# Kernel tuning notes

Measured on AMD Instinct MI355X. Metric: run time of the kernel, lower is better.

Reference implementation:

```python
import jax, jax.numpy as jnp
import numpy as np

B, N, D = 8, 2048, 1024


def setup_inputs() -> dict:
    key = jax.random.key(0)
    k = jax.random.split(key, 6)
    scale = 1.0 / np.sqrt(D)
    x = jax.random.normal(k[0], (B, N, D), dtype=jnp.float32)
    attention_mask = jax.random.randint(k[1], (B, N, N), 0, 2, dtype=jnp.int32)
    W_qkv = jax.random.normal(k[2], (D, 3 * D), dtype=jnp.float32) * scale
    b_qkv = jax.random.normal(k[3], (3 * D,), dtype=jnp.float32) * 0.01
    W_out = jax.random.normal(k[4], (D, D), dtype=jnp.float32) * scale
    b_out = jax.random.normal(k[5], (D,), dtype=jnp.float32) * 0.01
    return {"x": x, "attention_mask": attention_mask, "W_qkv": W_qkv,
            "b_qkv": b_qkv, "W_out": W_out, "b_out": b_out}


def reference(x, attention_mask, W_qkv, b_qkv, W_out, b_out):
    # QKV projection: [B,N,3D]
    qkv = jnp.einsum('bnd,de->bne', x, W_qkv) + b_qkv
    Q, K, V = jnp.split(qkv, 3, axis=-1)
    inv_sqrt_d = jnp.float32(1.0 / np.sqrt(D))
    # naive full [B,N,N] attention scores
    scores = jnp.einsum('bqd,bkd->bqk', Q, K) * inv_sqrt_d
    w = jax.nn.softmax(scores, axis=-1)
    # masked_fill(mask == 0, -1e20) then renormalize (module applies softmax
    # again over the masked weights; dropout is identity in eval mode)
    w = jnp.where(attention_mask == 0, jnp.float32(-1e20), w)
    w = jax.nn.softmax(w, axis=-1)
    out = jnp.einsum('bqk,bkd->bqd', w, V)
    return jnp.einsum('bnd,de->bne', out, W_out) + b_out
```

## Files before the change

kernel.cpp:

```cpp
#include <hip/hip_runtime.h>
#include <hip/hip_bf16.h>

typedef __attribute__((ext_vector_type(8))) short short8;
typedef __attribute__((ext_vector_type(4))) float floatx4;
typedef __attribute__((ext_vector_type(8))) int intx8;

#define AS_GLOBAL(p) ((const __attribute__((address_space(1))) void*)(p))
#define AS_LOCAL(p)  ((__attribute__((address_space(3))) void*)(p))

__device__ __forceinline__ float b2f(unsigned short u) {
    union { unsigned int u; float f; } c; c.u = ((unsigned int)u) << 16; return c.f;
}
__device__ __forceinline__ unsigned short f2b(float f) {
    union { float f; unsigned int u; } c; c.f = f;
    unsigned int u = c.u;
    unsigned int r = (u + 0x7fffu + ((u >> 16) & 1u)) >> 16;
    return (unsigned short)r;
}
__device__ __forceinline__ unsigned char f2fp8(float v) {
    return (unsigned char)(__builtin_amdgcn_cvt_pk_fp8_f32(v, v, 0, false) & 0xff);
}

__global__ __launch_bounds__(256) void cast_x(
    const float* __restrict__ in, unsigned short* __restrict__ xbf,
    unsigned int* __restrict__ xf8, int n4) {
    int i = blockIdx.x * 256 + threadIdx.x;
    if (i >= n4) return;
    float4 v = ((const float4*)in)[i];
    ushort4 o;
    o.x = f2b(v.x); o.y = f2b(v.y); o.z = f2b(v.z); o.w = f2b(v.w);
    ((ushort4*)xbf)[i] = o;
    int p = __builtin_amdgcn_cvt_pk_fp8_f32(v.x, v.y, 0, false);
    p = __builtin_amdgcn_cvt_pk_fp8_f32(v.z, v.w, p, true);
    xf8[i] = (unsigned int)p;
}

__global__ __launch_bounds__(256) void transpose_f32_bf16(
    const float* __restrict__ in, unsigned short* __restrict__ out, int R, int C) {
    __shared__ float t[32][33];
    int c0 = blockIdx.x * 32, r0 = blockIdx.y * 32;
    int tx = threadIdx.x, ty = threadIdx.y;
#pragma unroll
    for (int k = 0; k < 32; k += 8)
        t[ty + k][tx] = in[(size_t)(r0 + ty + k) * C + c0 + tx];
    __syncthreads();
#pragma unroll
    for (int k = 0; k < 32; k += 8)
        out[(size_t)(c0 + ty + k) * R + r0 + tx] = f2b(t[tx][ty + k]);
}

__global__ __launch_bounds__(256) void transpose_f32_fp8_qk(
    const float* __restrict__ in, unsigned char* __restrict__ out) {
    __shared__ float t[32][33];
    int c0 = blockIdx.x * 32, r0 = blockIdx.y * 32;
    int tx = threadIdx.x, ty = threadIdx.y;
#pragma unroll
    for (int k = 0; k < 32; k += 8)
        t[ty + k][tx] = in[(size_t)(r0 + ty + k) * 3072 + c0 + tx];
    __syncthreads();
#pragma unroll
    for (int k = 0; k < 32; k += 8)
        out[(size_t)(c0 + ty + k) * 1024 + r0 + tx] = f2fp8(t[tx][ty + k]);
}

__global__ __launch_bounds__(256) void cast_wv(
    const float* __restrict__ in, unsigned short* __restrict__ out) {
    int i = blockIdx.x * 256 + threadIdx.x;
    int d = i >> 8, rem = (i & 255) * 4;
    float4 v = *(const float4*)&in[(size_t)d * 3072 + 2048 + rem];
    ushort4 o;
    o.x = f2b(v.x); o.y = f2b(v.y); o.z = f2b(v.z); o.w = f2b(v.w);
    *(ushort4*)&out[(size_t)d * 1024 + rem] = o;
}

__global__ __launch_bounds__(256) void bvo_kernel(
    const unsigned short* __restrict__ WoT, const float* __restrict__ bqkv,
    const float* __restrict__ bout, float* __restrict__ bvo) {
    int wv = threadIdx.x >> 6, lane = threadIdx.x & 63;
    int e = blockIdx.x * 4 + wv;
    const unsigned short* row = WoT + (size_t)e * 1024;
    float s = 0.f;
    for (int h = lane; h < 1024; h += 64) s += b2f(row[h]) * bqkv[2048 + h];
#pragma unroll
    for (int o = 32; o; o >>= 1) s += __shfl_xor(s, o);
    if (lane == 0) bvo[e] = s + bout[e];
}

__global__ __launch_bounds__(256) void softmax2_kernel(
    unsigned short* __restrict__ S, const int* __restrict__ mask) {
    const int N = 2048;
    int wv = threadIdx.x >> 6, lane = threadIdx.x & 63;
    size_t row = (size_t)blockIdx.x * 4 + wv;
    unsigned short* srow = S + row * N;
    const int* mrow = mask + row * N;

    float e1[32];
    float l = 0.f;
#pragma unroll
    for (int i = 0; i < 4; ++i) {
        uint4 raw = ((const uint4*)srow)[lane + 64 * i];
        unsigned v[4] = { raw.x, raw.y, raw.z, raw.w };
#pragma unroll
        for (int j = 0; j < 4; ++j) {
            float a = b2f((unsigned short)(v[j] & 0xffff));
            float bb = b2f((unsigned short)(v[j] >> 16));
            float ea = __expf(a), eb = __expf(bb);
            e1[i * 8 + 2 * j] = ea; e1[i * 8 + 2 * j + 1] = eb;
            l += ea + eb;
        }
    }
#pragma unroll
    for (int o = 32; o; o >>= 1) l += __shfl_xor(l, o);
    float invl = 1.0f / l;

    float e2[32];
    float z = 0.f;
#pragma unroll
    for (int i = 0; i < 4; ++i) {
        uint4 m0 = ((const uint4*)mrow)[2 * (lane + 64 * i)];
        uint4 m1 = ((const uint4*)mrow)[2 * (lane + 64 * i) + 1];
        int mk[8] = { (int)m0.x, (int)m0.y, (int)m0.z, (int)m0.w,
                      (int)m1.x, (int)m1.y, (int)m1.z, (int)m1.w };
#pragma unroll
        for (int j = 0; j < 8; ++j) {
            float w1 = e1[i * 8 + j] * invl;
            float e = mk[j] ? __expf(w1) : 0.0f;
            e2[i * 8 + j] = e; z += e;
        }
    }
#pragma unroll
    for (int o = 32; o; o >>= 1) z += __shfl_xor(z, o);
    float invz = (z > 0.f) ? 1.0f / z : 0.0f;
    float fallback = 1.0f / N;
#pragma unroll
    for (int i = 0; i < 4; ++i) {
        float p[8];
#pragma unroll
        for (int j = 0; j < 8; ++j)
            p[j] = (z > 0.f) ? e2[i * 8 + j] * invz : fallback;
        uint4 o;
        o.x = (unsigned)f2b(p[0]) | ((unsigned)f2b(p[1]) << 16);
        o.y = (unsigned)f2b(p[2]) | ((unsigned)f2b(p[3]) << 16);
        o.z = (unsigned)f2b(p[4]) | ((unsigned)f2b(p[5]) << 16);
        o.w = (unsigned)f2b(p[6]) | ((unsigned)f2b(p[7]) << 16);
        ((uint4*)srow)[lane + 64 * i] = o;
    }
}

template <int TAG, bool BIAS, int OUT, int XS, int YS>
__global__ __launch_bounds__(256) void gemm_bt(
    const unsigned short* __restrict__ A, int ldA, long long strideA,
    const unsigned short* __restrict__ B, int ldB, long long strideB,
    void* __restrict__ C, int ldC, long long strideC,
    const float* __restrict__ bias, float scale, int K) {
    __shared__ __align__(16) unsigned short lds[2 * 128 * 64];
    unsigned short* At = lds;
    unsigned short* Bt = lds + 128 * 64;

    unsigned flat = blockIdx.x;
    unsigned wg = (flat & 7u) * (gridDim.x >> 3) + (flat >> 3);
    int bx = wg & ((1u << XS) - 1u);
    int by = (wg >> XS) & ((1u << YS) - 1u);
    int bz = wg >> (XS + YS);

    const unsigned short* Ab = A + (size_t)bz * strideA;
    const unsigned short* Bb = B + (size_t)bz * strideB;
    int tn0 = bx * 128;
    int tm0 = by * 128;
    int tid = threadIdx.x;
    int wave = tid >> 6, lane = tid & 63;
    int lm = lane & 15, q = lane >> 4;
    int wm = (wave >> 1) * 64, wn = (wave & 1) * 64;

    int srow = lane >> 3;
    int sblk = lane & 7;

    floatx4 acc[4][4] = {};

    for (int k0 = 0; k0 < K; k0 += 64) {
        __syncthreads();
#pragma unroll
        for (int i = 0; i < 4; ++i) {
            int chunk = wave * 4 + i;
            int r = chunk * 8 + srow;
            int blk = sblk ^ (r & 7);
            const unsigned short* ga = Ab + (size_t)(tm0 + r) * ldA + (k0 + blk * 8);
            __builtin_amdgcn_global_load_lds(AS_GLOBAL(ga), AS_LOCAL(At + chunk * 512), 16, 0, 0);
            const unsigned short* gb = Bb + (size_t)(tn0 + r) * ldB + (k0 + blk * 8);
            __builtin_amdgcn_global_load_lds(AS_GLOBAL(gb), AS_LOCAL(Bt + chunk * 512), 16, 0, 0);
        }
        __syncthreads();
#pragma unroll
        for (int kk = 0; kk < 2; ++kk) {
            short8 af[4], bf[4];
#pragma unroll
            for (int mt = 0; mt < 4; ++mt) {
                int r = wm + mt * 16 + lm;
                af[mt] = *(const short8*)(At + r * 64 + (((kk * 4 + q) ^ (r & 7)) * 8));
            }
#pragma unroll
            for (int nt = 0; nt < 4; ++nt) {
                int r = wn + nt * 16 + lm;
                bf[nt] = *(const short8*)(Bt + r * 64 + (((kk * 4 + q) ^ (r & 7)) * 8));
            }
#pragma unroll
            for (int mt = 0; mt < 4; ++mt)
#pragma unroll
                for (int nt = 0; nt < 4; ++nt)
                    acc[mt][nt] = __builtin_amdgcn_mfma_f32_16x16x32_bf16(
                        af[mt], bf[nt], acc[mt][nt], 0, 0, 0);
        }
    }

    float biasv[4];
#pragma unroll
    for (int nt = 0; nt < 4; ++nt)
        biasv[nt] = BIAS ? bias[tn0 + wn + nt * 16 + lm] : 0.0f;

    if (OUT == 2) {
        __syncthreads();
        unsigned short* T = lds;
#pragma unroll
        for (int mt = 0; mt < 4; ++mt)
#pragma unroll
            for (int nt = 0; nt < 4; ++nt) {
                int n = wn + nt * 16 + lm;
                int m0 = wm + mt * 16 + q * 4;
                int col = m0 ^ ((n & 15) << 3);
                ushort4 pv;
                float v0 = acc[mt][nt][0] * scale; if (BIAS) v0 += biasv[nt];
                float v1 = acc[mt][nt][1] * scale; if (BIAS) v1 += biasv[nt];
                float v2 = acc[mt][nt][2] * scale; if (BIAS) v2 += biasv[nt];
                float v3 = acc[mt][nt][3] * scale; if (BIAS) v3 += biasv[nt];
                pv.x = f2b(v0); pv.y = f2b(v1); pv.z = f2b(v2); pv.w = f2b(v3);
                *(ushort4*)&T[n * 128 + col] = pv;
            }
        __syncthreads();
        unsigned short* Cb = (unsigned short*)C + (size_t)(tm0 >> 11) * strideC + (tm0 & 2047);
#pragma unroll
        for (int r8 = 0; r8 < 8; ++r8) {
            int idx = tid + 256 * r8;
            int d = idx >> 4, c = idx & 15;
            int cs = (c ^ (d & 15)) << 3;
            short8 v = *(const short8*)&T[d * 128 + cs];
            *(short8*)&Cb[(size_t)(tn0 + d) * ldC + c * 8] = v;
        }
        return;
    }

#pragma unroll
    for (int mt = 0; mt < 4; ++mt) {
#pragma unroll
        for (int nt = 0; nt < 4; ++nt) {
            int gm = tm0 + wm + mt * 16 + q * 4;
            int gn = tn0 + wn + nt * 16 + lm;
#pragma unroll
            for (int r = 0; r < 4; ++r) {
                float v = acc[mt][nt][r] * scale;
                if (BIAS) v += biasv[nt];
                size_t idx = (size_t)bz * strideC + (size_t)(gm + r) * ldC + gn;
                if (OUT == 1) ((float*)C)[idx] = v;
                else          ((unsigned short*)C)[idx] = f2b(v);
            }
        }
    }
}

template <int MH>
__device__ __forceinline__ void mfma16(floatx4 (&acc)[8][4], const short8 (&af)[4],
                                       const short8 (&bf)[4]) {
#pragma unroll
    for (int m = 0; m < 4; ++m)
#pragma unroll
        for (int n = 0; n < 4; ++n)
            acc[MH * 4 + m][n] = __builtin_amdgcn_mfma_f32_16x16x32_bf16(
                af[m], bf[n], acc[MH * 4 + m][n], 0, 0, 0);
}

template <int NXB, int NYB>
__global__ __launch_bounds__(512, 2) void gemm_bt8(
    const unsigned short* __restrict__ A, int ldA, long long strideA,
    const unsigned short* __restrict__ B, int ldB, long long strideB,
    float* __restrict__ C, int ldC, long long strideC,
    float scale, int K) {
    __shared__ __align__(16) unsigned short lds[65536];
    constexpr int TILE = 16384;
    constexpr int BREG = 32768;

    int tid = threadIdx.x;
    int wave = tid >> 6, lane = tid & 63;
    int lm = lane & 15, q = lane >> 4;
    int wmi = wave >> 2, wni = wave & 3;

    unsigned flat = blockIdx.x;
    unsigned wg = (flat & 7u) * (gridDim.x >> 3) + (flat >> 3);
    int bx = wg % NXB;
    int rem = wg / NXB;
    int by = rem % NYB;
    int bz = rem / NYB;
    int tn0 = bx * 256, tm0 = by * 256;

    const unsigned short* Ab = A + (size_t)bz * strideA;
    const unsigned short* Bb = B + (size_t)bz * strideB;

    int srow8 = lane >> 3, s7 = lane & 7;
    const unsigned short* gA[4];
    const unsigned short* gB[4];
#pragma unroll
    for (int i = 0; i < 4; ++i) {
        int r = i * 64 + wave * 8 + srow8;
        int blk = s7 ^ (r & 7);
        gA[i] = Ab + (size_t)(tm0 + r) * ldA + blk * 8;
        gB[i] = Bb + (size_t)(tn0 + r) * ldB + blk * 8;
    }

    int nt = K >> 6;

#pragma unroll
    for (int i = 0; i < 4; ++i)
        __builtin_amdgcn_global_load_lds(AS_GLOBAL(gB[i]), AS_LOCAL(lds + BREG + i * 4096 + wave * 512), 16, 0, 0);
#pragma unroll
    for (int i = 0; i < 4; ++i)
        __builtin_amdgcn_global_load_lds(AS_GLOBAL(gA[i]), AS_LOCAL(lds + i * 4096 + wave * 512), 16, 0, 0);
#pragma unroll
    for (int i = 0; i < 4; ++i) { gA[i] += 64; gB[i] += 64; }

    asm volatile("s_waitcnt vmcnt(0)" ::: "memory");
    __builtin_amdgcn_s_barrier();

    floatx4 acc[8][4] = {};
    short8 bf0[4], bf1[4];
    short8 af[4];

    int aOff = (wmi * 128 + lm) * 64;
    int bOff = (wni * 64 + lm) * 64;
    int sl0 = (q ^ (lm & 7)) * 8;
    int sl1 = ((4 + q) ^ (lm & 7)) * 8;

    for (int t = 0; t < nt; ++t) {
        unsigned short* Ap = lds + (t & 1) * TILE;
        unsigned short* Bp = lds + BREG + (t & 1) * TILE;
        unsigned short* An = lds + ((t + 1) & 1) * TILE;
        unsigned short* Bn = lds + BREG + ((t + 1) & 1) * TILE;
        bool pre = (t + 1) < nt;

#pragma unroll
        for (int n = 0; n < 4; ++n) bf0[n] = *(const short8*)(Bp + bOff + n * 1024 + sl0);
#pragma unroll
        for (int n = 0; n < 4; ++n) bf1[n] = *(const short8*)(Bp + bOff + n * 1024 + sl1);
#pragma unroll
        for (int m = 0; m < 4; ++m) af[m] = *(const short8*)(Ap + aOff + m * 1024 + sl0);
        if (pre) {
#pragma unroll
            for (int i = 0; i < 4; ++i)
                __builtin_amdgcn_global_load_lds(AS_GLOBAL(gB[i]), AS_LOCAL(Bn + i * 4096 + wave * 512), 16, 0, 0);
        }
        __builtin_amdgcn_sched_barrier(0);
        __builtin_amdgcn_s_barrier();
        asm volatile("s_waitcnt lgkmcnt(0)" ::: "memory");
        __builtin_amdgcn_sched_barrier(0);
        __builtin_amdgcn_s_setprio(1);
        mfma16<0>(acc, af, bf0);
        __builtin_amdgcn_s_setprio(0);
        __builtin_amdgcn_s_barrier();

#pragma unroll
        for (int m = 0; m < 4; ++m) af[m] = *(const short8*)(Ap + aOff + 4096 + m * 1024 + sl0);
        if (pre) {
#pragma unroll
            for (int i = 0; i < 4; ++i)
                __builtin_amdgcn_global_load_lds(AS_GLOBAL(gA[i]), AS_LOCAL(An + i * 4096 + wave * 512), 16, 0, 0);
#pragma unroll
            for (int i = 0; i < 4; ++i) { gA[i] += 64; gB[i] += 64; }
        }
        __builtin_amdgcn_sched_barrier(0);
        __builtin_amdgcn_s_barrier();
        asm volatile("s_waitcnt lgkmcnt(0)" ::: "memory");
        __builtin_amdgcn_sched_barrier(0);
        __builtin_amdgcn_s_setprio(1);
        mfma16<1>(acc, af, bf0);
        __builtin_amdgcn_s_setprio(0);
        __builtin_amdgcn_s_barrier();

#pragma unroll
        for (int m = 0; m < 4; ++m) af[m] = *(const short8*)(Ap + aOff + m * 1024 + sl1);
        __builtin_amdgcn_sched_barrier(0);
        __builtin_amdgcn_s_barrier();
        asm volatile("s_waitcnt lgkmcnt(0)" ::: "memory");
        __builtin_amdgcn_sched_barrier(0);
        __builtin_amdgcn_s_setprio(1);
        mfma16<0>(acc, af, bf1);
        __builtin_amdgcn_s_setprio(0);
        __builtin_amdgcn_s_barrier();

#pragma unroll
        for (int m = 0; m < 4; ++m) af[m] = *(const short8*)(Ap + aOff + 4096 + m * 1024 + sl1);
        __builtin_amdgcn_sched_barrier(0);
        __builtin_amdgcn_s_barrier();
        asm volatile("s_waitcnt lgkmcnt(0)" ::: "memory");
        __builtin_amdgcn_sched_barrier(0);
        __builtin_amdgcn_s_setprio(1);
        mfma16<1>(acc, af, bf1);
        __builtin_amdgcn_s_setprio(0);
        asm volatile("s_waitcnt vmcnt(0)" ::: "memory");
        __builtin_amdgcn_s_barrier();
    }

    float* Cb = C + (size_t)bz * strideC;
#pragma unroll
    for (int m = 0; m < 8; ++m) {
#pragma unroll
        for (int n = 0; n < 4; ++n) {
            int gm = tm0 + wmi * 128 + m * 16 + q * 4;
            int gn = tn0 + wni * 64 + n * 16 + lm;
#pragma unroll
            for (int r = 0; r < 4; ++r)
                Cb[(size_t)(gm + r) * ldC + gn] = acc[m][n][r] * scale;
        }
    }
}

template <int TAG, bool BIAS, bool OUTFP8, int XS, int YS>
__global__ __launch_bounds__(256) void gemm_f8_bt(
    const unsigned char* __restrict__ A, int ldA, long long strideA,
    const unsigned char* __restrict__ B, int ldB, long long strideB,
    void* __restrict__ C, int ldC, long long strideC,
    const float* __restrict__ bias, float scale, int K) {
    __shared__ __align__(16) unsigned char lds[2 * 128 * 128];
    unsigned char* At = lds;
    unsigned char* Bt = lds + 128 * 128;

    unsigned flat = blockIdx.x;
    unsigned wg = (flat & 7u) * (gridDim.x >> 3) + (flat >> 3);
    int bx = wg & ((1u << XS) - 1u);
    int by = (wg >> XS) & ((1u << YS) - 1u);
    int bz = wg >> (XS + YS);

    const unsigned char* Ab = A + (size_t)bz * strideA;
    const unsigned char* Bb = B + (size_t)bz * strideB;
    int tn0 = bx * 128;
    int tm0 = by * 128;
    int tid = threadIdx.x;
    int wave = tid >> 6, lane = tid & 63;
    int lm = lane & 15, q = lane >> 4;
    int q2 = q * 2;
    int wm = (wave >> 1) * 64, wn = (wave & 1) * 64;

    int srow = lane >> 3;
    int sblk = lane & 7;

    floatx4 acc[4][4] = {};

    for (int k0 = 0; k0 < K; k0 += 128) {
        __syncthreads();
#pragma unroll
        for (int i = 0; i < 4; ++i) {
            int chunk = wave * 4 + i;
            int r = chunk * 8 + srow;
            int blk = sblk ^ (r & 7);
            const unsigned char* ga = Ab + (size_t)(tm0 + r) * ldA + (k0 + blk * 16);
            __builtin_amdgcn_global_load_lds(AS_GLOBAL(ga), AS_LOCAL(At + chunk * 1024), 16, 0, 0);
            const unsigned char* gb = Bb + (size_t)(tn0 + r) * ldB + (k0 + blk * 16);
            __builtin_amdgcn_global_load_lds(AS_GLOBAL(gb), AS_LOCAL(Bt + chunk * 1024), 16, 0, 0);
        }
        __syncthreads();
        intx8 af[4], bf[4];
#pragma unroll
        for (int mt = 0; mt < 4; ++mt) {
            int r = wm + mt * 16 + lm;
            const unsigned char* base = At + r * 128;
            int4 lo = *(const int4*)(base + ((q2 ^ (r & 7)) << 4));
            int4 hi = *(const int4*)(base + (((q2 + 1) ^ (r & 7)) << 4));
            af[mt][0] = lo.x; af[mt][1] = lo.y; af[mt][2] = lo.z; af[mt][3] = lo.w;
            af[mt][4] = hi.x; af[mt][5] = hi.y; af[mt][6] = hi.z; af[mt][7] = hi.w;
        }
#pragma unroll
        for (int nt = 0; nt < 4; ++nt) {
            int r = wn + nt * 16 + lm;
            const unsigned char* base = Bt + r * 128;
            int4 lo = *(const int4*)(base + ((q2 ^ (r & 7)) << 4));
            int4 hi = *(const int4*)(base + (((q2 + 1) ^ (r & 7)) << 4));
            bf[nt][0] = lo.x; bf[nt][1] = lo.y; bf[nt][2] = lo.z; bf[nt][3] = lo.w;
            bf[nt][4] = hi.x; bf[nt][5] = hi.y; bf[nt][6] = hi.z; bf[nt][7] = hi.w;
        }
#pragma unroll
        for (int mt = 0; mt < 4; ++mt)
#pragma unroll
            for (int nt = 0; nt < 4; ++nt)
                acc[mt][nt] = __builtin_amdgcn_mfma_scale_f32_16x16x128_f8f6f4(
                    af[mt], bf[nt], acc[mt][nt], 0, 0,
                    0, 0x7f7f7f7f, 0, 0x7f7f7f7f);
    }

    float biasv[4];
#pragma unroll
    for (int nt = 0; nt < 4; ++nt)
        biasv[nt] = BIAS ? bias[tn0 + wn + nt * 16 + lm] : 0.0f;
#pragma unroll
    for (int mt = 0; mt < 4; ++mt) {
#pragma unroll
        for (int nt = 0; nt < 4; ++nt) {
            int gm = tm0 + wm + mt * 16 + q * 4;
            int gn = tn0 + wn + nt * 16 + lm;
#pragma unroll
            for (int r = 0; r < 4; ++r) {
                float v = acc[mt][nt][r] * scale;
                if (BIAS) v += biasv[nt];
                size_t idx = (size_t)bz * strideC + (size_t)(gm + r) * ldC + gn;
                if (OUTFP8) ((unsigned char*)C)[idx] = f2fp8(v);
                else        ((unsigned short*)C)[idx] = f2b(v);
            }
        }
    }
}

extern "C" void kernel_launch(void* const* d_in, const int* in_sizes, int n_in,
                              void* d_out, int out_size, void* d_ws, size_t ws_size,
                              hipStream_t stream) {
    const float* x    = (const float*)d_in[0];
    const int*   mask = (const int*)d_in[1];
    const float* Wqkv = (const float*)d_in[2];
    const float* bqkv = (const float*)d_in[3];
    const float* Wout = (const float*)d_in[4];
    const float* bout = (const float*)d_in[5];
    float* out = (float*)d_out;

    char* w = (char*)d_ws;
    unsigned short* x_bf  = (unsigned short*)(w);
    unsigned char*  x_f8  = (unsigned char*)(w + 33554432);
    unsigned char*  QKf8  = (unsigned char*)(w + 50331648);
    unsigned short* VpT   = (unsigned short*)(w + 117440512);
    unsigned short* S     = (unsigned short*)(w + 150994944);
    unsigned char*  WqkT8 = (unsigned char*)(w + 218103808);
    unsigned short* WoT   = (unsigned short*)(w + 220200960);
    unsigned short* Wv_bf = (unsigned short*)(w + 222298112);
    unsigned short* WvoT  = (unsigned short*)(w + 224395264);
    float*          bvo   = (float*)(w + 226492416);

    cast_x<<<16384, 256, 0, stream>>>(x, x_bf, (unsigned int*)x_f8, 4194304);
    transpose_f32_fp8_qk<<<dim3(64, 32), dim3(32, 8), 0, stream>>>(Wqkv, WqkT8);
    transpose_f32_bf16<<<dim3(32, 32), dim3(32, 8), 0, stream>>>(Wout, WoT, 1024, 1024);
    cast_wv<<<1024, 256, 0, stream>>>(Wqkv, Wv_bf);
    bvo_kernel<<<256, 256, 0, stream>>>(WoT, bqkv, bout, bvo);

    gemm_bt<4, false, 0, 3, 3><<<64, 256, 0, stream>>>(
        WoT, 1024, 0, Wv_bf, 1024, 0, WvoT, 1024, 0, nullptr, 1.0f, 1024);

    gemm_f8_bt<0, true, true, 4, 7><<<2048, 256, 0, stream>>>(
        x_f8, 1024, 0, WqkT8, 1024, 0, QKf8, 2048, 0, bqkv, 1.0f, 1024);

    gemm_bt<5, true, 2, 3, 7><<<1024, 256, 0, stream>>>(
        x_bf, 1024, 0, WvoT, 1024, 0, VpT, 2048, 1024LL * 2048, bvo, 1.0f, 1024);

    gemm_f8_bt<1, false, false, 4, 4><<<2048, 256, 0, stream>>>(
        QKf8, 2048, 2048LL * 2048, QKf8 + 1024, 2048, 2048LL * 2048,
        S, 2048, 2048LL * 2048, nullptr, 0.03125f, 1024);

    softmax2_kernel<<<4096, 256, 0, stream>>>(S, mask);

    gemm_bt8<4, 8><<<256, 512, 0, stream>>>(
        S, 2048, 2048LL * 2048, VpT, 2048, 1024LL * 2048,
        out, 1024, 2048LL * 1024, 1.0f, 2048);
}
```

Before: 500.3 us.

## Replace FP8 GEMM with 256x256-tile double-buffered 8-wave pipelined kernel

Replaces the 128x128 single-buffered FP8 GEMM used for the QK projection and the QK^T scores with a 256x256-tile, 512-thread kernel. It double-buffers A and B tiles in 128KB of LDS and splits each K-step into two half-tile MFMA phases, issuing global-to-LDS prefetch of the next tile between them. It also uses s_setprio around the MFMA blocks. The aim is to hide global-load latency and raise data reuse per tile. In exchange it uses a large LDS footprint and more accumulator registers, which limits occupancy, and the grid drops to 512 blocks.

```diff
diff --git a/kernel.cpp b/kernel.cpp
--- a/kernel.cpp
+++ b/kernel.cpp
@@ -420,92 +420,142 @@
     }
 }
 
-template <int TAG, bool BIAS, bool OUTFP8, int XS, int YS>
-__global__ __launch_bounds__(256) void gemm_f8_bt(
+__device__ __forceinline__ void rd_f8(intx8& d, const unsigned char* p, int lo, int hi) {
+    int4 L = *(const int4*)(p + lo);
+    int4 H = *(const int4*)(p + hi);
+    d[0] = L.x; d[1] = L.y; d[2] = L.z; d[3] = L.w;
+    d[4] = H.x; d[5] = H.y; d[6] = H.z; d[7] = H.w;
+}
+
+template <bool BIAS, bool OUTFP8, int NXB, int NYB>
+__global__ __launch_bounds__(512, 2) void gemm_f8_bt8(
     const unsigned char* __restrict__ A, int ldA, long long strideA,
     const unsigned char* __restrict__ B, int ldB, long long strideB,
     void* __restrict__ C, int ldC, long long strideC,
     const float* __restrict__ bias, float scale, int K) {
-    __shared__ __align__(16) unsigned char lds[2 * 128 * 128];
-    unsigned char* At = lds;
-    unsigned char* Bt = lds + 128 * 128;
-
-    unsigned flat = blockIdx.x;
-    unsigned wg = (flat & 7u) * (gridDim.x >> 3) + (flat >> 3);
-    int bx = wg & ((1u << XS) - 1u);
-    int by = (wg >> XS) & ((1u << YS) - 1u);
-    int bz = wg >> (XS + YS);
-
-    const unsigned char* Ab = A + (size_t)bz * strideA;
-    const unsigned char* Bb = B + (size_t)bz * strideB;
-    int tn0 = bx * 128;
-    int tm0 = by * 128;
+    __shared__ __align__(16) unsigned char lds[131072];
+    constexpr int TILE = 32768;
+    constexpr int BREG = 65536;
+
     int tid = threadIdx.x;
     int wave = tid >> 6, lane = tid & 63;
     int lm = lane & 15, q = lane >> 4;
     int q2 = q * 2;
-    int wm = (wave >> 1) * 64, wn = (wave & 1) * 64;
-
-    int srow = lane >> 3;
-    int sblk = lane & 7;
-
-    floatx4 acc[4][4] = {};
-
-    for (int k0 = 0; k0 < K; k0 += 128) {
-        __syncthreads();
-#pragma unroll
-        for (int i = 0; i < 4; ++i) {
-            int chunk = wave * 4 + i;
-            int r = chunk * 8 + srow;
-            int blk = sblk ^ (r & 7);
-            const unsigned char* ga = Ab + (size_t)(tm0 + r) * ldA + (k0 + blk * 16);
-            __builtin_amdgcn_global_load_lds(AS_GLOBAL(ga), AS_LOCAL(At + chunk * 1024), 16, 0, 0);
-            const unsigned char* gb = Bb + (size_t)(tn0 + r) * ldB + (k0 + blk * 16);
-            __builtin_amdgcn_global_load_lds(AS_GLOBAL(gb), AS_LOCAL(Bt + chunk * 1024), 16, 0, 0);
-        }
-        __syncthreads();
-        intx8 af[4], bf[4];
-#pragma unroll
-        for (int mt = 0; mt < 4; ++mt) {
-            int r = wm + mt * 16 + lm;
-            const unsigned char* base = At + r * 128;
-            int4 lo = *(const int4*)(base + ((q2 ^ (r & 7)) << 4));
-            int4 hi = *(const int4*)(base + (((q2 + 1) ^ (r & 7)) << 4));
-            af[mt][0] = lo.x; af[mt][1] = lo.y; af[mt][2] = lo.z; af[mt][3] = lo.w;
-            af[mt][4] = hi.x; af[mt][5] = hi.y; af[mt][6] = hi.z; af[mt][7] = hi.w;
-        }
-#pragma unroll
-        for (int nt = 0; nt < 4; ++nt) {
-            int r = wn + nt * 16 + lm;
-            const unsigned char* base = Bt + r * 128;
-            int4 lo = *(const int4*)(base + ((q2 ^ (r & 7)) << 4));
-            int4 hi = *(const int4*)(base + (((q2 + 1) ^ (r & 7)) << 4));
-            bf[nt][0] = lo.x; bf[nt][1] = lo.y; bf[nt][2] = lo.z; bf[nt][3] = lo.w;
-            bf[nt][4] = hi.x; bf[nt][5] = hi.y; bf[nt][6] = hi.z; bf[nt][7] = hi.w;
-        }
-#pragma unroll
-        for (int mt = 0; mt < 4; ++mt)
-#pragma unroll
-            for (int nt = 0; nt < 4; ++nt)
-                acc[mt][nt] = __builtin_amdgcn_mfma_scale_f32_16x16x128_f8f6f4(
-                    af[mt], bf[nt], acc[mt][nt], 0, 0,
-                    0, 0x7f7f7f7f, 0, 0x7f7f7f7f);
+    int wmi = wave >> 2, wni = wave & 3;
+
+    unsigned flat = blockIdx.x;
+    unsigned wg = (flat & 7u) * (gridDim.x >> 3) + (flat >> 3);
+    int bx = wg % NXB;
+    int rem = wg / NXB;
+    int by = rem % NYB;
+    int bz = rem / NYB;
+    int tn0 = bx * 256, tm0 = by * 256;
+
+    const unsigned char* Ab = A + (size_t)bz * strideA;
+    const unsigned char* Bb = B + (size_t)bz * strideB;
+
+    int srow8 = lane >> 3, s7 = lane & 7;
+    const unsigned char* gA[4];
+    const unsigned char* gB[4];
+#pragma unroll
+    for (int i = 0; i < 4; ++i) {
+        int r = i * 64 + wave * 8 + srow8;
+        int blk = s7 ^ (r & 7);
+        gA[i] = Ab + (size_t)(tm0 + r) * ldA + blk * 16;
+        gB[i] = Bb + (size_t)(tn0 + r) * ldB + blk * 16;
+    }
+
+    int nt = K >> 7;
+
+#pragma unroll
+    for (int i = 0; i < 4; ++i)
+        __builtin_amdgcn_global_load_lds(AS_GLOBAL(gB[i]), AS_LOCAL(lds + BREG + i * 8192 + wave * 1024), 16, 0, 0);
+#pragma unroll
+    for (int i = 0; i < 4; ++i)
+        __builtin_amdgcn_global_load_lds(AS_GLOBAL(gA[i]), AS_LOCAL(lds + i * 8192 + wave * 1024), 16, 0, 0);
+#pragma unroll
+    for (int i = 0; i < 4; ++i) { gA[i] += 128; gB[i] += 128; }
+
+    asm volatile("s_waitcnt vmcnt(0)" ::: "memory");
+    __builtin_amdgcn_s_barrier();
+
+    floatx4 acc[8][4] = {};
+    intx8 afr[4], bfr[4];
+
+    int aOff = (wmi * 128 + lm) * 128;
+    int bOff = (wni * 64 + lm) * 128;
+    int lo = (q2 ^ (lm & 7)) << 4;
+    int hi = ((q2 + 1) ^ (lm & 7)) << 4;
+
+    for (int t = 0; t < nt; ++t) {
+        unsigned char* Ap = lds + (t & 1) * TILE;
+        unsigned char* Bp = lds + BREG + (t & 1) * TILE;
+        unsigned char* An = lds + ((t + 1) & 1) * TILE;
+        unsigned char* Bn = lds + BREG + ((t + 1) & 1) * TILE;
+        bool pre = (t + 1) < nt;
+
+#pragma unroll
+        for (int n = 0; n < 4; ++n) rd_f8(bfr[n], Bp + bOff + n * 2048, lo, hi);
+#pragma unroll
+        for (int m = 0; m < 4; ++m) rd_f8(afr[m], Ap + aOff + m * 2048, lo, hi);
+        if (pre) {
+#pragma unroll
+            for (int i = 0; i < 4; ++i)
+                __builtin_amdgcn_global_load_lds(AS_GLOBAL(gB[i]), AS_LOCAL(Bn + i * 8192 + wave * 1024), 16, 0, 0);
+        }
+        __builtin_amdgcn_sched_barrier(0);
+        __builtin_amdgcn_s_barrier();
+        asm volatile("s_waitcnt lgkmcnt(0)" ::: "memory");
+        __builtin_amdgcn_sched_barrier(0);
+        __builtin_amdgcn_s_setprio(1);
+#pragma unroll
+        for (int m = 0; m < 4; ++m)
+#pragma unroll
+            for (int n = 0; n < 4; ++n)
+                acc[m][n] = __builtin_amdgcn_mfma_scale_f32_16x16x128_f8f6f4(
+                    afr[m], bfr[n], acc[m][n], 0, 0, 0, 0x7f7f7f7f, 0, 0x7f7f7f7f);
+        __builtin_amdgcn_s_setprio(0);
+        __builtin_amdgcn_s_barrier();
+
+#pragma unroll
+        for (int m = 0; m < 4; ++m) rd_f8(afr[m], Ap + aOff + 8192 + m * 2048, lo, hi);
+        if (pre) {
+#pragma unroll
+            for (int i = 0; i < 4; ++i)
+                __builtin_amdgcn_global_load_lds(AS_GLOBAL(gA[i]), AS_LOCAL(An + i * 8192 + wave * 1024), 16, 0, 0);
+#pragma unroll
+            for (int i = 0; i < 4; ++i) { gA[i] += 128; gB[i] += 128; }
+        }
+        __builtin_amdgcn_sched_barrier(0);
+        __builtin_amdgcn_s_barrier();
+        asm volatile("s_waitcnt lgkmcnt(0)" ::: "memory");
+        __builtin_amdgcn_sched_barrier(0);
+        __builtin_amdgcn_s_setprio(1);
+#pragma unroll
+        for (int m = 0; m < 4; ++m)
+#pragma unroll
+            for (int n = 0; n < 4; ++n)
+                acc[4 + m][n] = __builtin_amdgcn_mfma_scale_f32_16x16x128_f8f6f4(
+                    afr[m], bfr[n], acc[4 + m][n], 0, 0, 0, 0x7f7f7f7f, 0, 0x7f7f7f7f);
+        __builtin_amdgcn_s_setprio(0);
+        asm volatile("s_waitcnt vmcnt(0)" ::: "memory");
+        __builtin_amdgcn_s_barrier();
     }
 
     float biasv[4];
 #pragma unroll
-    for (int nt = 0; nt < 4; ++nt)
-        biasv[nt] = BIAS ? bias[tn0 + wn + nt * 16 + lm] : 0.0f;
-#pragma unroll
-    for (int mt = 0; mt < 4; ++mt) {
-#pragma unroll
-        for (int nt = 0; nt < 4; ++nt) {
-            int gm = tm0 + wm + mt * 16 + q * 4;
-            int gn = tn0 + wn + nt * 16 + lm;
+    for (int n = 0; n < 4; ++n)
+        biasv[n] = BIAS ? bias[tn0 + wni * 64 + n * 16 + lm] : 0.0f;
+#pragma unroll
+    for (int m = 0; m < 8; ++m) {
+#pragma unroll
+        for (int n = 0; n < 4; ++n) {
+            int gm = tm0 + wmi * 128 + m * 16 + q * 4;
+            int gn = tn0 + wni * 64 + n * 16 + lm;
 #pragma unroll
             for (int r = 0; r < 4; ++r) {
-                float v = acc[mt][nt][r] * scale;
-                if (BIAS) v += biasv[nt];
+                float v = acc[m][n][r] * scale;
+                if (BIAS) v += biasv[n];
                 size_t idx = (size_t)bz * strideC + (size_t)(gm + r) * ldC + gn;
                 if (OUTFP8) ((unsigned char*)C)[idx] = f2fp8(v);
                 else        ((unsigned short*)C)[idx] = f2b(v);
@@ -546,13 +596,13 @@
     gemm_bt<4, false, 0, 3, 3><<<64, 256, 0, stream>>>(
         WoT, 1024, 0, Wv_bf, 1024, 0, WvoT, 1024, 0, nullptr, 1.0f, 1024);
 
-    gemm_f8_bt<0, true, true, 4, 7><<<2048, 256, 0, stream>>>(
+    gemm_f8_bt8<true, true, 8, 64><<<512, 512, 0, stream>>>(
         x_f8, 1024, 0, WqkT8, 1024, 0, QKf8, 2048, 0, bqkv, 1.0f, 1024);
 
     gemm_bt<5, true, 2, 3, 7><<<1024, 256, 0, stream>>>(
         x_bf, 1024, 0, WvoT, 1024, 0, VpT, 2048, 1024LL * 2048, bvo, 1.0f, 1024);
 
-    gemm_f8_bt<1, false, false, 4, 4><<<2048, 256, 0, stream>>>(
+    gemm_f8_bt8<false, false, 8, 8><<<512, 512, 0, stream>>>(
         QKf8, 2048, 2048LL * 2048, QKf8 + 1024, 2048, 2048LL * 2048,
         S, 2048, 2048LL * 2048, nullptr, 0.03125f, 1024);
 
```

Measured after the change: 499.3 us. Within noise of the previous version (-0.2%).
